# Kernel tuning notes

Hardware: AMD Instinct MI355X
Metric: run time of the kernel (lower is better)

Reference implementation:

```python
import jax, jax.numpy as jnp
import numpy as np

EMBED = 1024
HEADS = 16
HEAD_DIM = EMBED // HEADS
FF = 4096
LN_EPS = 1e-5


def _layer_norm(x, scale, bias):
    mu = jnp.mean(x, axis=-1, keepdims=True)
    var = jnp.mean(jnp.square(x - mu), axis=-1, keepdims=True)
    return (x - mu) * jax.lax.rsqrt(var + LN_EPS) * scale + bias


def setup_inputs() -> dict:
    key = jax.random.key(0)
    ks = jax.random.split(key, 16)
    B, T, CARRY = 8, 128, 4096
    s = 0.02
    return {
        "hidden": jax.random.normal(ks[0], (B, T, EMBED), jnp.float32),
        "key_carry": jax.random.normal(ks[1], (B, HEADS, CARRY, HEAD_DIM), jnp.float32),
        "value_carry": jax.random.normal(ks[2], (B, HEADS, CARRY, HEAD_DIM), jnp.float32),
        "ln1_scale": jnp.ones((EMBED,), jnp.float32),
        "ln1_bias": jnp.zeros((EMBED,), jnp.float32),
        "wq": jax.random.normal(ks[3], (EMBED, EMBED), jnp.float32) * s,
        "bq": jnp.zeros((EMBED,), jnp.float32),
        "wk": jax.random.normal(ks[4], (EMBED, EMBED), jnp.float32) * s,
        "bk": jnp.zeros((EMBED,), jnp.float32),
        "wv": jax.random.normal(ks[5], (EMBED, EMBED), jnp.float32) * s,
        "bv": jnp.zeros((EMBED,), jnp.float32),
        "wo": jax.random.normal(ks[6], (EMBED, EMBED), jnp.float32) * s,
        "bo": jnp.zeros((EMBED,), jnp.float32),
        "ln2_scale": jnp.ones((EMBED,), jnp.float32),
        "ln2_bias": jnp.zeros((EMBED,), jnp.float32),
        "w1": jax.random.normal(ks[7], (EMBED, FF), jnp.float32) * s,
        "b1": jnp.zeros((FF,), jnp.float32),
        "w2": jax.random.normal(ks[8], (FF, EMBED), jnp.float32) * s,
        "b2": jnp.zeros((EMBED,), jnp.float32),
    }


def reference(hidden, key_carry, value_carry, ln1_scale, ln1_bias, wq, bq, wk, bk,
              wv, bv, wo, bo, ln2_scale, ln2_bias, w1, b1, w2, b2):
    B, T, _ = hidden.shape
    carry_len = key_carry.shape[2]

    x = _layer_norm(hidden, ln1_scale, ln1_bias)
    # [B, H, T, Dh]
    def split_heads(y):
        return y.reshape(B, T, HEADS, HEAD_DIM).transpose(0, 2, 1, 3)
    q = split_heads(x @ wq + bq)
    k = split_heads(x @ wk + bk)
    v = split_heads(x @ wv + bv)

    k_all = jnp.concatenate([key_carry, k], axis=2)   # [B,H,C+T,Dh]
    v_all = jnp.concatenate([value_carry, v], axis=2)

    scores = jnp.einsum("bhtd,bhsd->bhts", q, k_all) / jnp.sqrt(jnp.float32(HEAD_DIM))
    kv_pos = jnp.arange(carry_len + T)
    q_pos = jnp.arange(T)[:, None] + carry_len
    causal = kv_pos[None, :] <= q_pos  # [T, C+T]
    scores = jnp.where(causal[None, None], scores, jnp.float32(-jnp.inf))
    attn = jax.nn.softmax(scores, axis=-1)  # dropout=0.0 (eval)
    ctx = jnp.einsum("bhts,bhsd->bhtd", attn, v_all)
    ctx = ctx.transpose(0, 2, 1, 3).reshape(B, T, EMBED)
    hidden = hidden + (ctx @ wo + bo)

    f = _layer_norm(hidden, ln2_scale, ln2_bias)
    f = jax.nn.gelu(f @ w1 + b1, approximate=False) @ w2 + b2
    hidden = hidden + f
    return hidden, k_all, v_all
```

## Files before the change

kernel.cpp:

```cpp
#include <hip/hip_runtime.h>
#include <hip/hip_bf16.h>
#include <math.h>

#define EMBED 1024
#define HEADS 16
#define HDIM 64
#define FFDIM 4096
#define BATCH 8
#define TLEN 128
#define CARRY 4096
#define SEQA (CARRY + TLEN)
#define MROWS (BATCH * TLEN)
#define NSPLIT 8

typedef __attribute__((ext_vector_type(8))) short bf16x8;
typedef __attribute__((ext_vector_type(4))) float f32x4;
typedef unsigned short u16;

static __device__ __forceinline__ u16 f2b(float v) {
    __hip_bfloat16 h = __float2bfloat16(v);
    return *reinterpret_cast<u16*>(&h);
}

typedef const __attribute__((address_space(1))) unsigned int g_u32;
// ... 109 lines not shown
        float4 v = *(const float4*)(W + (size_t)(k0 + r) * N + n0 + c);
        Ls[r][c] = v.x; Ls[r][c + 1] = v.y; Ls[r][c + 2] = v.z; Ls[r][c + 3] = v.w;
    }
    __syncthreads();
#pragma unroll
    for (int p = 0; p < 4; p++) {
        int n = (tid >> 4) + 16 * p, k4 = (tid & 15) * 4;
        u16 o0 = f2b(Ls[k4][n]), o1 = f2b(Ls[k4 + 1][n]);
        u16 o2 = f2b(Ls[k4 + 2][n]), o3 = f2b(Ls[k4 + 3][n]);
        unsigned int a = (unsigned int)o0 | ((unsigned int)o1 << 16);
        unsigned int b = (unsigned int)o2 | ((unsigned int)o3 << 16);
        uint2 pk = {a, b};
        *(uint2*)(WT + (size_t)(n0 + n) * K + k0 + k4) = pk;
    }
}

static __device__ __forceinline__ void stage2(const u16* __restrict__ Ag,
                                              const u16* __restrict__ Wg,
                                              u16* As, u16* Ws,
                                              int w, int l, int K) {
    int r0 = 16 * w + (l >> 3);
    int scol = ((l & 7) ^ (l >> 3)) * 8;
    char* a0 = (char*)As + w * 2048;
    char* w0 = (char*)Ws + w * 2048;
    gl16(Ag + (size_t)r0 * K + scol, a0);
    gl16(Ag + (size_t)(r0 + 8) * K + scol, a0 + 1024);
    gl16(Wg + (size_t)r0 * K + scol, w0);
    gl16(Wg + (size_t)(r0 + 8) * K + scol, w0 + 1024);
}

template <int MODE>
__global__ __launch_bounds__(256) void gemm_bf16(const u16* __restrict__ A,
                                                 const u16* __restrict__ WT,
                                                 const float* __restrict__ bias,
                                                 const float* __restrict__ resid,
                                                 float* __restrict__ outf,
                                                 float* __restrict__ outf2,
                                                 u16* __restrict__ outb, int N, int K) {
    __shared__ u16 As[64 * 64];
    __shared__ u16 Ws[64 * 64];
    int tid = threadIdx.x;
    int m0 = blockIdx.y * 64, n0 = blockIdx.x * 64;
    int w = tid >> 6, l = tid & 63, lr = l & 15, lg = l >> 4;
    f32x4 acc[4] = {};

    const u16* Ag = A + (size_t)m0 * K;
    const u16* Wg = WT + (size_t)n0 * K;

    for (int k0 = 0; k0 < K; k0 += 64) {
        __syncthreads();
        stage2(Ag + k0, Wg + k0, As, Ws, w, l, K);
        __syncthreads();
#pragma unroll
        for (int ks = 0; ks < 2; ks++) {
            int abyte = ((16 * w + lr) * 128 + lg * 16 + ks * 64) ^ ((lr & 7) << 4);
            bf16x8 af = *(bf16x8*)((char*)As + abyte);
#pragma unroll
            for (int f = 0; f < 4; f++) {
                int bbyte = ((16 * f + lr) * 128 + lg * 16 + ks * 64) ^ ((lr & 7) << 4);
                bf16x8 bfr = *(bf16x8*)((char*)Ws + bbyte);
                acc[f] = __builtin_amdgcn_mfma_f32_16x16x32_bf16(af, bfr, acc[f], 0, 0, 0);
            }
        }
    }

    int gr0 = m0 + 16 * w + 4 * lg;
#pragma unroll
    for (int f = 0; f < 4; f++) {
        int gc = n0 + 16 * f + lr;
        float bv = bias[gc];
#pragma unroll
        for (int r = 0; r < 4; r++) {
            int gm = gr0 + r;
            float v = acc[f][r] + bv;
            if (MODE == 3) v = 0.5f * v * (1.0f + erff(v * 0.70710678118654752f));
            if (MODE == 2 || MODE == 4) v += resid[(size_t)gm * EMBED + gc];
            if (MODE == 0 || MODE == 3) {
                outb[(size_t)gm * N + gc] = f2b(v);
            } else if (MODE == 1) {
                int b_ = gm >> 7, t_ = gm & 127, h_ = gc >> 6, d_ = gc & 63;
                outf[(((size_t)(b_ * HEADS + h_)) * SEQA + CARRY + t_) * HDIM + d_] = v;
            } else if (MODE == 5) {
                if (gc < 1024) {
                    outb[(size_t)gm * EMBED + gc] = f2b(v);
                } else {
                    int which = gc >> 10;
                    int gc2 = gc & 1023;
                    int b_ = gm >> 7, t_ = gm & 127, h_ = gc2 >> 6, d_ = gc2 & 63;
                    float* dst = (which == 1) ? outf : outf2;
                    dst[(((size_t)(b_ * HEADS + h_)) * SEQA + CARRY + t_) * HDIM + d_] = v;
                }
            } else {
                outf[(size_t)gm * EMBED + gc] = v;
            }
        }
    }
}

__global__ __launch_bounds__(256) void gemm_splitk(const u16* __restrict__ A,
                                                   const u16* __restrict__ WT,
                                                   float* __restrict__ part,
                                                   int N, int Ktot, int Klen) {
    __shared__ u16 As[64 * 64];
    __shared__ u16 Ws[64 * 64];
    int tid = threadIdx.x;
    int m0 = blockIdx.y * 64, n0 = blockIdx.x * 64;
    int k0s = blockIdx.z * Klen;
    int w = tid >> 6, l = tid & 63, lr = l & 15, lg = l >> 4;
    f32x4 acc[4] = {};

    const u16* Ag = A + (size_t)m0 * Ktot;
    const u16* Wg = WT + (size_t)n0 * Ktot;

    for (int k0 = k0s; k0 < k0s + Klen; k0 += 64) {
        __syncthreads();
        stage2(Ag + k0, Wg + k0, As, Ws, w, l, Ktot);
        __syncthreads();
#pragma unroll
        for (int ks = 0; ks < 2; ks++) {
            int abyte = ((16 * w + lr) * 128 + lg * 16 + ks * 64) ^ ((lr & 7) << 4);
            bf16x8 af = *(bf16x8*)((char*)As + abyte);
#pragma unroll
            for (int f = 0; f < 4; f++) {
                int bbyte = ((16 * f + lr) * 128 + lg * 16 + ks * 64) ^ ((lr & 7) << 4);
                bf16x8 bfr = *(bf16x8*)((char*)Ws + bbyte);
                acc[f] = __builtin_amdgcn_mfma_f32_16x16x32_bf16(af, bfr, acc[f], 0, 0, 0);
            }
        }
    }

    float* pbase = part + (size_t)blockIdx.z * MROWS * N;
    int gr0 = m0 + 16 * w + 4 * lg;
#pragma unroll
    for (int f = 0; f < 4; f++) {
        int gc = n0 + 16 * f + lr;
#pragma unroll
        for (int r = 0; r < 4; r++)
            pbase[(size_t)(gr0 + r) * N + gc] = acc[f][r];
    }
}

template <int NS>
__global__ __launch_bounds__(256) void combine_add(const float* __restrict__ part,
                                                   const float* __restrict__ bias,
                                                   const float* __restrict__ resid,
                                                   float* __restrict__ out) {
    size_t e = ((size_t)blockIdx.x * 256 + threadIdx.x) * 4;
    int n0 = (int)(e & 1023);
    float4 v = *(const float4*)(resid + e);
    float4 b = *(const float4*)(bias + n0);
    v.x += b.x; v.y += b.y; v.z += b.z; v.w += b.w;
#pragma unroll
    for (int s = 0; s < NS; s++) {
        float4 p = *(const float4*)(part + (size_t)s * MROWS * EMBED + e);
        v.x += p.x; v.y += p.y; v.z += p.z; v.w += p.w;
    }
    *(float4*)(out + e) = v;
}

__global__ __launch_bounds__(256) void combine_ln(const float* __restrict__ part,
                                                  const float* __restrict__ bias,
                                                  const float* __restrict__ resid,
                                                  const float* __restrict__ ln_s,
                                                  const float* __restrict__ ln_b,
                                                  float* __restrict__ out,
                                                  u16* __restrict__ outb) {
    int row = blockIdx.x, tid = threadIdx.x;
    size_t base = (size_t)row * EMBED + tid * 4;
    float4 v = *(const float4*)(resid + base);
    float4 b = *(const float4*)(bias + tid * 4);
    v.x += b.x; v.y += b.y; v.z += b.z; v.w += b.w;
#pragma unroll
    for (int s = 0; s < 2; s++) {
        float4 p = *(const float4*)(part + (size_t)s * MROWS * EMBED + base);
        v.x += p.x; v.y += p.y; v.z += p.z; v.w += p.w;
    }
    *(float4*)(out + base) = v;

    float s1 = v.x + v.y + v.z + v.w;
    float s2 = v.x * v.x + v.y * v.y + v.z * v.z + v.w * v.w;
    for (int o = 32; o > 0; o >>= 1) {
        s1 += __shfl_down(s1, o, 64);
        s2 += __shfl_down(s2, o, 64);
    }
    __shared__ float ls[8], ls2[8];
    int wid = tid >> 6, lane = tid & 63;
    if (lane == 0) { ls[wid] = s1; ls2[wid] = s2; }
    __syncthreads();
    if (tid == 0) {
        float S = 0.f, S2 = 0.f;
        for (int i = 0; i < 4; i++) { S += ls[i]; S2 += ls2[i]; }
        float mu = S * (1.0f / EMBED);
        float var = S2 * (1.0f / EMBED) - mu * mu;
        ls[0] = mu;
        ls2[0] = rsqrtf(var + 1e-5f);
    }
    __syncthreads();
    float mu = ls[0], rstd = ls2[0];
    float sc[4], bi[4];
    *(float4*)sc = ((const float4*)ln_s)[tid];
    *(float4*)bi = ((const float4*)ln_b)[tid];
    u16 o0 = f2b((v.x - mu) * rstd * sc[0] + bi[0]);
    u16 o1 = f2b((v.y - mu) * rstd * sc[1] + bi[1]);
    u16 o2 = f2b((v.z - mu) * rstd * sc[2] + bi[2]);
    u16 o3 = f2b((v.w - mu) * rstd * sc[3] + bi[3]);
    unsigned int u0 = (unsigned int)o0 | ((unsigned int)o1 << 16);
    unsigned int u1 = (unsigned int)o2 | ((unsigned int)o3 << 16);
    uint2 pk = {u0, u1};
    *(uint2*)(outb + base) = pk;
}

__global__ __launch_bounds__(256) void attn_mfma_split(const u16* __restrict__ qb,
                                                       const float* __restrict__ kc,
                                                       const float* __restrict__ vc,
                                                       float* __restrict__ k_all,
                                                       float* __restrict__ v_all,
                                                       float* __restrict__ part_acc,
                                                       float* __restrict__ part_m,
                                                       float* __restrict__ part_l) {
    __shared__ u16 Ks[64 * 64];
    __shared__ u16 Vt[64 * 64];
    __shared__ u16 Ps[64 * 64];

    int bh = blockIdx.x, b = bh >> 4, h = bh & 15;
    int qh = blockIdx.y;
    int q0 = qh * 64;
    int sp = blockIdx.z;
    int tid = threadIdx.x;
    int w = tid >> 6, l = tid & 63, lr = l & 15, lg = l >> 4;
    const bool WR = (qh == 0);

    bf16x8 qf0, qf1;
    {
        const u16* qrow = qb + (size_t)(b * TLEN + q0 + 16 * w + lr) * EMBED + h * HDIM;
        qf0 = *(const bf16x8*)(qrow + 8 * lg);
        qf1 = *(const bf16x8*)(qrow + 8 * lg + 32);
    }

    const float* kcb = kc + (size_t)bh * CARRY * HDIM;
    const float* vcb = vc + (size_t)bh * CARRY * HDIM;
    const float* kb = k_all + (size_t)bh * SEQA * HDIM;
    const float* vb = v_all + (size_t)bh * SEQA * HDIM;
    float* kwr = k_all + (size_t)bh * SEQA * HDIM;
    float* vwr = v_all + (size_t)bh * SEQA * HDIM;

    float m_run[4], l_run[4];
    f32x4 oacc[4] = {};
#pragma unroll
    for (int r = 0; r < 4; r++) { m_run[r] = -1e30f; l_run[r] = 0.f; }

    int nt = (CARRY + q0 + 64) >> 6;
    int tps = (nt + NSPLIT - 1) / NSPLIT;
    int kt0 = sp * tps;
    int kt1 = min(kt0 + tps, nt);

    int krow = tid >> 4;
    int vrow4 = (tid >> 4) * 4;
    int col = (tid & 15) * 4;

    float4 kA[4], vA[4], kB[4], vB[4];

    {
        bool cn = kt0 < 64;
        const float* ksrc = cn ? kcb : kb;
        const float* vsrc = cn ? vcb : vb;
#pragma unroll
        for (int p = 0; p < 4; p++)
            kA[p] = *(const float4*)(ksrc + (size_t)(kt0 * 64 + krow + 16 * p) * HDIM + col);
#pragma unroll
        for (int p = 0; p < 4; p++)
            vA[p] = *(const float4*)(vsrc + (size_t)(kt0 * 64 + vrow4 + p) * HDIM + col);
    }

    auto body = [&](float4 (&kc_)[4], float4 (&vc_)[4],
                    float4 (&kn_)[4], float4 (&vn_)[4], int kt) {
        bool carry_t = kt < 64;
        int ktn = kt + 1;
        if (ktn < kt1) {
            bool cn = ktn < 64;
            const float* ksrc = cn ? kcb : kb;
            const float* vsrc = cn ? vcb : vb;
#pragma unroll
            for (int p = 0; p < 4; p++)
                kn_[p] = *(const float4*)(ksrc + (size_t)(ktn * 64 + krow + 16 * p) * HDIM + col);
#pragma unroll
            for (int p = 0; p < 4; p++)
                vn_[p] = *(const float4*)(vsrc + (size_t)(ktn * 64 + vrow4 + p) * HDIM + col);
        }
        if (WR && carry_t) {
#pragma unroll
            for (int p = 0; p < 4; p++)
                *(float4*)(kwr + (size_t)(kt * 64 + krow + 16 * p) * HDIM + col) = kc_[p];
#pragma unroll
            for (int p = 0; p < 4; p++)
                *(float4*)(vwr + (size_t)(kt * 64 + vrow4 + p) * HDIM + col) = vc_[p];
        }
        bar_plain();
#pragma unroll
        for (int p = 0; p < 4; p++) {
            int s = krow + 16 * p;
            u16 t0 = f2b(kc_[p].x), t1 = f2b(kc_[p].y), t2 = f2b(kc_[p].z), t3 = f2b(kc_[p].w);
            unsigned int a = (unsigned int)t0 | ((unsigned int)t1 << 16);
            unsigned int bq = (unsigned int)t2 | ((unsigned int)t3 << 16);
            uint2 pk = {a, bq};
            *(uint2*)((char*)Ks + ((s * 128 + col * 2) ^ ((s & 7) << 4))) = pk;
        }
#pragma unroll
        for (int i = 0; i < 4; i++) {
            int d = col + i;
            u16 e0 = f2b(((const float*)&vc_[0])[i]);
            u16 e1 = f2b(((const float*)&vc_[1])[i]);
            u16 e2 = f2b(((const float*)&vc_[2])[i]);
            u16 e3 = f2b(((const float*)&vc_[3])[i]);
            unsigned int a = (unsigned int)e0 | ((unsigned int)e1 << 16);
            unsigned int bq = (unsigned int)e2 | ((unsigned int)e3 << 16);
            uint2 pk = {a, bq};
            *(uint2*)((char*)Vt + ((d * 128 + vrow4 * 2) ^ ((d & 7) << 4))) = pk;
        }
        bar_lgkm();

        float x[4][4];
#pragma unroll
        for (int f = 0; f < 4; f++) {
            int row = 16 * f + lr;
            int swz = (row & 7) << 4;
            bf16x8 kf0 = *(bf16x8*)((char*)Ks + ((row * 128 + 16 * lg) ^ swz));
            bf16x8 kf1 = *(bf16x8*)((char*)Ks + ((row * 128 + 16 * lg + 64) ^ swz));
            f32x4 z = {};
            z = __builtin_amdgcn_mfma_f32_16x16x32_bf16(qf0, kf0, z, 0, 0, 0);
            z = __builtin_amdgcn_mfma_f32_16x16x32_bf16(qf1, kf1, z, 0, 0, 0);
#pragma unroll
            for (int r = 0; r < 4; r++) x[f][r] = z[r] * 0.125f;
        }
        if (kt * 64 + 63 > CARRY + q0 + 16 * w) {
#pragma unroll
            for (int f = 0; f < 4; f++) {
                int sg = kt * 64 + 16 * f + lr;
#pragma unroll
                for (int r = 0; r < 4; r++) {
                    int tg = q0 + 16 * w + 4 * lg + r;
                    if (sg > CARRY + tg) x[f][r] = -1e30f;
                }
            }
        }
#pragma unroll
        for (int r = 0; r < 4; r++) {
            float mt = fmaxf(fmaxf(x[0][r], x[1][r]), fmaxf(x[2][r], x[3][r]));
            mt = fmaxf(mt, __shfl_xor(mt, 1, 64));
            mt = fmaxf(mt, __shfl_xor(mt, 2, 64));
            mt = fmaxf(mt, __shfl_xor(mt, 4, 64));
            mt = fmaxf(mt, __shfl_xor(mt, 8, 64));
            float mn = fmaxf(m_run[r], mt);
            float fs = __expf(m_run[r] - mn);
            m_run[r] = mn;
            float s = 0.f;
#pragma unroll
            for (int f = 0; f < 4; f++) {
                float p = __expf(x[f][r] - mn);
                x[f][r] = p;
                s += p;
            }
            s += __shfl_xor(s, 1, 64);
            s += __shfl_xor(s, 2, 64);
            s += __shfl_xor(s, 4, 64);
            s += __shfl_xor(s, 8, 64);
            l_run[r] = l_run[r] * fs + s;
#pragma unroll
            for (int f2 = 0; f2 < 4; f2++) oacc[f2][r] *= fs;
        }
#pragma unroll
        for (int f = 0; f < 4; f++) {
#pragma unroll
            for (int r = 0; r < 4; r++) {
                int row = 16 * w + 4 * lg + r;
                int byte = (row * 128 + (16 * f + lr) * 2) ^ ((row & 7) << 4);
                *(u16*)((char*)Ps + byte) = f2b(x[f][r]);
            }
        }
        {
            int prow = 16 * w + lr;
            int pswz = (prow & 7) << 4;
            bf16x8 pa0 = *(bf16x8*)((char*)Ps + ((prow * 128 + 16 * lg) ^ pswz));
            bf16x8 pa1 = *(bf16x8*)((char*)Ps + ((prow * 128 + 16 * lg + 64) ^ pswz));
#pragma unroll
            for (int f2 = 0; f2 < 4; f2++) {
                int d = 16 * f2 + lr;
                int vswz = (d & 7) << 4;
                bf16x8 vf0 = *(bf16x8*)((char*)Vt + ((d * 128 + 16 * lg) ^ vswz));
                bf16x8 vf1 = *(bf16x8*)((char*)Vt + ((d * 128 + 16 * lg + 64) ^ vswz));
                oacc[f2] = __builtin_amdgcn_mfma_f32_16x16x32_bf16(pa0, vf0, oacc[f2], 0, 0, 0);
                oacc[f2] = __builtin_amdgcn_mfma_f32_16x16x32_bf16(pa1, vf1, oacc[f2], 0, 0, 0);
            }
        }
    };

    for (int kt = kt0; kt < kt1; kt += 2) {
        body(kA, vA, kB, vB, kt);
        if (kt + 1 < kt1) body(kB, vB, kA, vA, kt + 1);
    }

    int p = (bh * 2 + qh) * NSPLIT + sp;
    if (lr == 0) {
#pragma unroll
        for (int r = 0; r < 4; r++) {
            int row = 16 * w + 4 * lg + r;
            part_m[(size_t)p * 64 + row] = m_run[r];
            part_l[(size_t)p * 64 + row] = l_run[r];
        }
    }
#pragma unroll
    for (int f2 = 0; f2 < 4; f2++) {
#pragma unroll
        for (int r = 0; r < 4; r++) {
            int row = 16 * w + 4 * lg + r;
            part_acc[(size_t)p * 4096 + row * 64 + 16 * f2 + lr] = oacc[f2][r];
        }
    }
}

__global__ __launch_bounds__(256) void attn_combine(const float* __restrict__ part_acc,
                                                    const float* __restrict__ part_m,
                                                    const float* __restrict__ part_l,
                                                    u16* __restrict__ ctx) {
    int g = blockIdx.x;
    int bh = g >> 1, qh = g & 1, b = bh >> 4, h = bh & 15;
    int t = threadIdx.x;
    int r = t >> 2, c0 = (t & 3) * 16;
    int p0 = g * NSPLIT;

    float ms[NSPLIT];
    float M = -1e30f;
#pragma unroll
    for (int s = 0; s < NSPLIT; s++) {
        ms[s] = part_m[(size_t)(p0 + s) * 64 + r];
        M = fmaxf(M, ms[s]);
    }
    float wgt[NSPLIT];
    float L = 0.f;
#pragma unroll
    for (int s = 0; s < NSPLIT; s++) {
        wgt[s] = __expf(ms[s] - M);
        L += wgt[s] * part_l[(size_t)(p0 + s) * 64 + r];
    }
    float inv = 1.0f / L;

    size_t grow = (size_t)(b * TLEN + qh * 64 + r) * EMBED + h * HDIM + c0;
#pragma unroll
    for (int j = 0; j < 16; j += 4) {
        float4 a = {0.f, 0.f, 0.f, 0.f};
#pragma unroll
        for (int s = 0; s < NSPLIT; s++) {
            float4 p = *(const float4*)(part_acc + (size_t)(p0 + s) * 4096 + r * 64 + c0 + j);
            a.x += wgt[s] * p.x; a.y += wgt[s] * p.y; a.z += wgt[s] * p.z; a.w += wgt[s] * p.w;
        }
        u16 o0 = f2b(a.x * inv), o1 = f2b(a.y * inv), o2 = f2b(a.z * inv), o3 = f2b(a.w * inv);
        unsigned int u0 = (unsigned int)o0 | ((unsigned int)o1 << 16);
        unsigned int u1 = (unsigned int)o2 | ((unsigned int)o3 << 16);
        uint2 pk = {u0, u1};
        *(uint2*)(ctx + grow + j) = pk;
    }
}

__global__ __launch_bounds__(256) void attn_mfma(const u16* __restrict__ qb,
                                                 const float* __restrict__ k_all,
                                                 const float* __restrict__ v_all,
                                                 u16* __restrict__ ctx) {
    __shared__ u16 Ks[64 * 64];
    __shared__ u16 Vt[64 * 64];
    __shared__ u16 Ps[64 * 64];

    int bh = blockIdx.x, b = bh >> 4, h = bh & 15;
    int q0 = blockIdx.y * 64;
    int tid = threadIdx.x;
    int w = tid >> 6, l = tid & 63, lr = l & 15, lg = l >> 4;

    bf16x8 qf0, qf1;
    {
        const u16* qrow = qb + (size_t)(b * TLEN + q0 + 16 * w + lr) * EMBED + h * HDIM;
        qf0 = *(const bf16x8*)(qrow + 8 * lg);
        qf1 = *(const bf16x8*)(qrow + 8 * lg + 32);
    }
    const float* kb = k_all + (size_t)bh * SEQA * HDIM;
    const float* vb = v_all + (size_t)bh * SEQA * HDIM;

    float m_run[4], l_run[4];
    f32x4 oacc[4] = {};
#pragma unroll
    for (int r = 0; r < 4; r++) { m_run[r] = -1e30f; l_run[r] = 0.f; }

    int nt = (CARRY + q0 + 64) >> 6;
    for (int kt = 0; kt < nt; kt++) {
        __syncthreads();
#pragma unroll
        for (int p = 0; p < 4; p++) {
            int s = (tid >> 4) + 16 * p, c = (tid & 15) * 4;
            float4 kv = *(const float4*)(kb + (size_t)(kt * 64 + s) * HDIM + c);
            u16 t0 = f2b(kv.x), t1 = f2b(kv.y), t2 = f2b(kv.z), t3 = f2b(kv.w);
            unsigned int a = (unsigned int)t0 | ((unsigned int)t1 << 16);
            unsigned int bq = (unsigned int)t2 | ((unsigned int)t3 << 16);
            uint2 pk = {a, bq};
            int byte = (s * 128 + c * 2) ^ ((s & 7) << 4);
            *(uint2*)((char*)Ks + byte) = pk;
        }
        {
            int d = tid & 63;
            u16 tmp[16];
#pragma unroll
            for (int q = 0; q < 16; q++)
                tmp[q] = f2b(vb[(size_t)(kt * 64 + 16 * w + q) * HDIM + d]);
            int b0 = (d * 128 + 32 * w) ^ ((d & 7) << 4);
            int b1 = (d * 128 + 32 * w + 16) ^ ((d & 7) << 4);
            *(bf16x8*)((char*)Vt + b0) = *(bf16x8*)&tmp[0];
            *(bf16x8*)((char*)Vt + b1) = *(bf16x8*)&tmp[8];
        }
        __syncthreads();

        float x[4][4];
#pragma unroll
        for (int f = 0; f < 4; f++) {
            int row = 16 * f + lr;
            int swz = (row & 7) << 4;
            bf16x8 kf0 = *(bf16x8*)((char*)Ks + ((row * 128 + 16 * lg) ^ swz));
            bf16x8 kf1 = *(bf16x8*)((char*)Ks + ((row * 128 + 16 * lg + 64) ^ swz));
            f32x4 z = {};
            z = __builtin_amdgcn_mfma_f32_16x16x32_bf16(qf0, kf0, z, 0, 0, 0);
            z = __builtin_amdgcn_mfma_f32_16x16x32_bf16(qf1, kf1, z, 0, 0, 0);
#pragma unroll
            for (int r = 0; r < 4; r++) x[f][r] = z[r] * 0.125f;
        }
        if (kt * 64 + 63 > CARRY + q0 + 16 * w) {
#pragma unroll
            for (int f = 0; f < 4; f++) {
                int sg = kt * 64 + 16 * f + lr;
#pragma unroll
                for (int r = 0; r < 4; r++) {
// ... 21 lines not shown
            }
            s += __shfl_xor(s, 1, 64);
            s += __shfl_xor(s, 2, 64);
            s += __shfl_xor(s, 4, 64);
            s += __shfl_xor(s, 8, 64);
            l_run[r] = l_run[r] * fs + s;
#pragma unroll
            for (int f2 = 0; f2 < 4; f2++) oacc[f2][r] *= fs;
        }
#pragma unroll
        for (int f = 0; f < 4; f++) {
#pragma unroll
            for (int r = 0; r < 4; r++) {
                int row = 16 * w + 4 * lg + r;
                int byte = (row * 128 + (16 * f + lr) * 2) ^ ((row & 7) << 4);
                *(u16*)((char*)Ps + byte) = f2b(x[f][r]);
            }
        }
        {
            int prow = 16 * w + lr;
            int pswz = (prow & 7) << 4;
            bf16x8 pa0 = *(bf16x8*)((char*)Ps + ((prow * 128 + 16 * lg) ^ pswz));
            bf16x8 pa1 = *(bf16x8*)((char*)Ps + ((prow * 128 + 16 * lg + 64) ^ pswz));
#pragma unroll
            for (int f2 = 0; f2 < 4; f2++) {
                int d = 16 * f2 + lr;
                int vswz = (d & 7) << 4;
                bf16x8 vf0 = *(bf16x8*)((char*)Vt + ((d * 128 + 16 * lg) ^ vswz));
                bf16x8 vf1 = *(bf16x8*)((char*)Vt + ((d * 128 + 16 * lg + 64) ^ vswz));
                oacc[f2] = __builtin_amdgcn_mfma_f32_16x16x32_bf16(pa0, vf0, oacc[f2], 0, 0, 0);
                oacc[f2] = __builtin_amdgcn_mfma_f32_16x16x32_bf16(pa1, vf1, oacc[f2], 0, 0, 0);
            }
        }
    }
#pragma unroll
    for (int r = 0; r < 4; r++) {
        float inv = 1.0f / l_run[r];
        size_t grow = (size_t)(b * TLEN + q0 + 16 * w + 4 * lg + r) * EMBED + h * HDIM;
#pragma unroll
        for (int f2 = 0; f2 < 4; f2++)
            ctx[grow + 16 * f2 + lr] = f2b(oacc[f2][r] * inv);
    }
}

extern "C" void kernel_launch(void* const* d_in, const int* in_sizes, int n_in,
                              void* d_out, int out_size, void* d_ws, size_t ws_size,
                              hipStream_t stream) {
    const float* hidden = (const float*)d_in[0];
    const float* key_carry = (const float*)d_in[1];
    const float* value_carry = (const float*)d_in[2];
    const float* ln1_s = (const float*)d_in[3];
    const float* ln1_b = (const float*)d_in[4];
    const float* wq = (const float*)d_in[5];
    const float* bq = (const float*)d_in[6];
    const float* wk = (const float*)d_in[7];
    const float* bk = (const float*)d_in[8];
    const float* wv = (const float*)d_in[9];
    const float* bv = (const float*)d_in[10];
    const float* wo = (const float*)d_in[11];
    const float* bo = (const float*)d_in[12];
    const float* ln2_s = (const float*)d_in[13];
    const float* ln2_b = (const float*)d_in[14];
    const float* w1 = (const float*)d_in[15];
    const float* b1 = (const float*)d_in[16];
    const float* w2 = (const float*)d_in[17];
    const float* b2 = (const float*)d_in[18];

    float* out_hidden = (float*)d_out;
    float* k_all = out_hidden + (size_t)MROWS * EMBED;
    float* v_all = k_all + (size_t)BATCH * HEADS * SEQA * HDIM;

    u16* wsu = (u16*)d_ws;
    u16* wqkvT = wsu;
    u16* woT = wsu + 3145728;
    u16* w1T = wsu + 4194304;
    u16* w2T = wsu + 8388608;
    u16* xb  = wsu + 12582912;
    u16* qbb = wsu + 13631488;
    u16* ctxb = wsu + 14680064;
    u16* fb  = wsu + 15728640;
    u16* h1b = wsu + 16777216;
    float* bias_qkv = (float*)(wsu + 20971520);
    float* part = (float*)(wsu + 20977664);
    const size_t nparts = (size_t)256 * NSPLIT;
    const size_t need = (size_t)20977664 * 2 +
                        (nparts * 4096 + 2 * nparts * 64) * 4;

    transpose_all<<<dim3(16, 16, 12), 256, 0, stream>>>(wq, wk, wv, wo, w1, w2, bq, bk, bv,
                                                        wqkvT, woT, w1T, w2T, bias_qkv);

    ln_kernel<<<MROWS, 256, 0, stream>>>(hidden, ln1_s, ln1_b, xb);

    if (ws_size >= need) {
        gemm_bf16<5><<<dim3(48, 16), 256, 0, stream>>>(xb, wqkvT, bias_qkv, nullptr,
                                                       k_all, v_all, qbb, 3072, EMBED);
        float* part_acc = part;
        float* part_m = part + nparts * 4096;
        float* part_l = part_m + nparts * 64;
        attn_mfma_split<<<dim3(BATCH * HEADS, 2, NSPLIT), 256, 0, stream>>>(
            qbb, key_carry, value_carry, k_all, v_all, part_acc, part_m, part_l);
        attn_combine<<<256, 256, 0, stream>>>(part_acc, part_m, part_l, ctxb);

        gemm_splitk<<<dim3(16, 16, 2), 256, 0, stream>>>(ctxb, woT, part, EMBED, EMBED, 512);
        combine_ln<<<1024, 256, 0, stream>>>(part, bo, hidden, ln2_s, ln2_b, out_hidden, fb);

        gemm_bf16<3><<<dim3(64, 16), 256, 0, stream>>>(fb, w1T, b1, nullptr, nullptr, nullptr,
                                                       h1b, FFDIM, EMBED);
        gemm_splitk<<<dim3(16, 16, 4), 256, 0, stream>>>(h1b, w2T, part, EMBED, FFDIM, 1024);
        combine_add<4><<<1024, 256, 0, stream>>>(part, b2, out_hidden, out_hidden);
    } else {
        copy_carry_kernel<<<2048, 256, 0, stream>>>(
            (const float4*)key_carry, (const float4*)value_carry,
            (float4*)k_all, (float4*)v_all);
        u16* wqT = wqkvT;
        u16* wkT = wqkvT + 1048576;
        u16* wvT = wqkvT + 2097152;
        gemm_bf16<0><<<dim3(16, 16), 256, 0, stream>>>(xb, wqT, bq, nullptr, nullptr, nullptr,
                                                       qbb, EMBED, EMBED);
        gemm_bf16<1><<<dim3(16, 16), 256, 0, stream>>>(xb, wkT, bk, nullptr, k_all, nullptr,
                                                       nullptr, EMBED, EMBED);
        gemm_bf16<1><<<dim3(16, 16), 256, 0, stream>>>(xb, wvT, bv, nullptr, v_all, nullptr,
                                                       nullptr, EMBED, EMBED);
        attn_mfma<<<dim3(BATCH * HEADS, 2), 256, 0, stream>>>(qbb, k_all, v_all, ctxb);
        gemm_bf16<2><<<dim3(16, 16), 256, 0, stream>>>(ctxb, woT, bo, hidden, out_hidden,
                                                       nullptr, nullptr, EMBED, EMBED);
        ln_kernel<<<MROWS, 256, 0, stream>>>(out_hidden, ln2_s, ln2_b, fb);
        gemm_bf16<3><<<dim3(64, 16), 256, 0, stream>>>(fb, w1T, b1, nullptr, nullptr, nullptr,
                                                       h1b, FFDIM, EMBED);
        gemm_bf16<4><<<dim3(16, 16), 256, 0, stream>>>(h1b, w2T, b2, out_hidden, out_hidden,
                                                       nullptr, nullptr, EMBED, FFDIM);
    }
}
```

Measured before the change: 251.3 us.

## Process all 128 query rows per attention block to halve K/V loads

Result: slower. 289.0 us (+15.0%).

```diff
diff --git a/kernel.cpp b/kernel.cpp
--- a/kernel.cpp
+++ b/kernel.cpp
@@ -353,21 +353,19 @@
                                                        float* __restrict__ part_l) {
     __shared__ u16 Ks[64 * 64];
     __shared__ u16 Vt[64 * 64];
-    __shared__ u16 Ps[64 * 64];
+    __shared__ u16 Ps[128 * 64];
 
     int bh = blockIdx.x, b = bh >> 4, h = bh & 15;
-    int qh = blockIdx.y;
-    int q0 = qh * 64;
-    int sp = blockIdx.z;
+    int sp = blockIdx.y;
     int tid = threadIdx.x;
     int w = tid >> 6, l = tid & 63, lr = l & 15, lg = l >> 4;
-    const bool WR = (qh == 0);
-
-    bf16x8 qf0, qf1;
-    {
-        const u16* qrow = qb + (size_t)(b * TLEN + q0 + 16 * w + lr) * EMBED + h * HDIM;
-        qf0 = *(const bf16x8*)(qrow + 8 * lg);
-        qf1 = *(const bf16x8*)(qrow + 8 * lg + 32);
+
+    bf16x8 qf[2][2];
+#pragma unroll
+    for (int rr = 0; rr < 2; rr++) {
+        const u16* qrow = qb + (size_t)(b * TLEN + 32 * w + 16 * rr + lr) * EMBED + h * HDIM;
+        qf[rr][0] = *(const bf16x8*)(qrow + 8 * lg);
+        qf[rr][1] = *(const bf16x8*)(qrow + 8 * lg + 32);
     }
 
     const float* kcb = kc + (size_t)bh * CARRY * HDIM;
@@ -377,13 +375,15 @@
     float* kwr = k_all + (size_t)bh * SEQA * HDIM;
     float* vwr = v_all + (size_t)bh * SEQA * HDIM;
 
-    float m_run[4], l_run[4];
-    f32x4 oacc[4] = {};
-#pragma unroll
-    for (int r = 0; r < 4; r++) { m_run[r] = -1e30f; l_run[r] = 0.f; }
-
-    int nt = (CARRY + q0 + 64) >> 6;
-    int tps = (nt + NSPLIT - 1) / NSPLIT;
+    float m_run[2][4], l_run[2][4];
+    f32x4 oacc[2][4] = {};
+#pragma unroll
+    for (int rr = 0; rr < 2; rr++)
+#pragma unroll
+        for (int r = 0; r < 4; r++) { m_run[rr][r] = -1e30f; l_run[rr][r] = 0.f; }
+
+    const int nt = SEQA / 64;
+    const int tps = (nt + NSPLIT - 1) / NSPLIT;
     int kt0 = sp * tps;
     int kt1 = min(kt0 + tps, nt);
 
@@ -420,7 +420,7 @@
             for (int p = 0; p < 4; p++)
                 vn_[p] = *(const float4*)(vsrc + (size_t)(ktn * 64 + vrow4 + p) * HDIM + col);
         }
-        if (WR && carry_t) {
+        if (carry_t) {
 #pragma unroll
             for (int p = 0; p < 4; p++)
                 *(float4*)(kwr + (size_t)(kt * 64 + krow + 16 * p) * HDIM + col) = kc_[p];
@@ -452,66 +452,70 @@
         }
         bar_lgkm();
 
-        float x[4][4];
-#pragma unroll
-        for (int f = 0; f < 4; f++) {
-            int row = 16 * f + lr;
-            int swz = (row & 7) << 4;
-            bf16x8 kf0 = *(bf16x8*)((char*)Ks + ((row * 128 + 16 * lg) ^ swz));
-            bf16x8 kf1 = *(bf16x8*)((char*)Ks + ((row * 128 + 16 * lg + 64) ^ swz));
-            f32x4 z = {};
-            z = __builtin_amdgcn_mfma_f32_16x16x32_bf16(qf0, kf0, z, 0, 0, 0);
-            z = __builtin_amdgcn_mfma_f32_16x16x32_bf16(qf1, kf1, z, 0, 0, 0);
-#pragma unroll
-            for (int r = 0; r < 4; r++) x[f][r] = z[r] * 0.125f;
-        }
-        if (kt * 64 + 63 > CARRY + q0 + 16 * w) {
+#pragma unroll
+        for (int rr = 0; rr < 2; rr++) {
+            float x[4][4];
 #pragma unroll
             for (int f = 0; f < 4; f++) {
-                int sg = kt * 64 + 16 * f + lr;
+                int row = 16 * f + lr;
+                int swz = (row & 7) << 4;
+                bf16x8 kf0 = *(bf16x8*)((char*)Ks + ((row * 128 + 16 * lg) ^ swz));
+                bf16x8 kf1 = *(bf16x8*)((char*)Ks + ((row * 128 + 16 * lg + 64) ^ swz));
+                f32x4 z = {};
+                z = __builtin_amdgcn_mfma_f32_16x16x32_bf16(qf[rr][0], kf0, z, 0, 0, 0);
+                z = __builtin_amdgcn_mfma_f32_16x16x32_bf16(qf[rr][1], kf1, z, 0, 0, 0);
+#pragma unroll
+                for (int r = 0; r < 4; r++) x[f][r] = z[r] * 0.125f;
+            }
+            if (kt * 64 + 63 > CARRY + 32 * w + 16 * rr) {
+#pragma unroll
+                for (int f = 0; f < 4; f++) {
+                    int sg = kt * 64 + 16 * f + lr;
+#pragma unroll
+                    for (int r = 0; r < 4; r++) {
+                        int tg = 32 * w + 16 * rr + 4 * lg + r;
+                        if (sg > CARRY + tg) x[f][r] = -1e30f;
+                    }
+                }
+            }
+#pragma unroll
+            for (int r = 0; r < 4; r++) {
+                float mt = fmaxf(fmaxf(x[0][r], x[1][r]), fmaxf(x[2][r], x[3][r]));
+                mt = fmaxf(mt, __shfl_xor(mt, 1, 64));
+                mt = fmaxf(mt, __shfl_xor(mt, 2, 64));
+                mt = fmaxf(mt, __shfl_xor(mt, 4, 64));
+                mt = fmaxf(mt, __shfl_xor(mt, 8, 64));
+                float mn = fmaxf(m_run[rr][r], mt);
+                float fs = __expf(m_run[rr][r] - mn);
+                m_run[rr][r] = mn;
+                float s = 0.f;
+#pragma unroll
+                for (int f = 0; f < 4; f++) {
+                    float p = __expf(x[f][r] - mn);
+                    x[f][r] = p;
+                    s += p;
+                }
+                s += __shfl_xor(s, 1, 64);
+                s += __shfl_xor(s, 2, 64);
+                s += __shfl_xor(s, 4, 64);
+                s += __shfl_xor(s, 8, 64);
+                l_run[rr][r] = l_run[rr][r] * fs + s;
+#pragma unroll
+                for (int f2 = 0; f2 < 4; f2++) oacc[rr][f2][r] *= fs;
+            }
+#pragma unroll
+            for (int f = 0; f < 4; f++) {
 #pragma unroll
                 for (int r = 0; r < 4; r++) {
-                    int tg = q0 + 16 * w + 4 * lg + r;
-                    if (sg > CARRY + tg) x[f][r] = -1e30f;
+                    int row = 32 * w + 16 * rr + 4 * lg + r;
+                    int byte = (row * 128 + (16 * f + lr) * 2) ^ ((row & 7) << 4);
+                    *(u16*)((char*)Ps + byte) = f2b(x[f][r]);
                 }
             }
         }
 #pragma unroll
-        for (int r = 0; r < 4; r++) {
-            float mt = fmaxf(fmaxf(x[0][r], x[1][r]), fmaxf(x[2][r], x[3][r]));
-            mt = fmaxf(mt, __shfl_xor(mt, 1, 64));
-            mt = fmaxf(mt, __shfl_xor(mt, 2, 64));
-            mt = fmaxf(mt, __shfl_xor(mt, 4, 64));
-            mt = fmaxf(mt, __shfl_xor(mt, 8, 64));
-            float mn = fmaxf(m_run[r], mt);
-            float fs = __expf(m_run[r] - mn);
-            m_run[r] = mn;
-            float s = 0.f;
-#pragma unroll
-            for (int f = 0; f < 4; f++) {
-                float p = __expf(x[f][r] - mn);
-                x[f][r] = p;
-                s += p;
-            }
-            s += __shfl_xor(s, 1, 64);
-            s += __shfl_xor(s, 2, 64);
-            s += __shfl_xor(s, 4, 64);
-            s += __shfl_xor(s, 8, 64);
-            l_run[r] = l_run[r] * fs + s;
-#pragma unroll
-            for (int f2 = 0; f2 < 4; f2++) oacc[f2][r] *= fs;
-        }
-#pragma unroll
-        for (int f = 0; f < 4; f++) {
-#pragma unroll
-            for (int r = 0; r < 4; r++) {
-                int row = 16 * w + 4 * lg + r;
-                int byte = (row * 128 + (16 * f + lr) * 2) ^ ((row & 7) << 4);
-                *(u16*)((char*)Ps + byte) = f2b(x[f][r]);
-            }
-        }
-        {
-            int prow = 16 * w + lr;
+        for (int rr = 0; rr < 2; rr++) {
+            int prow = 32 * w + 16 * rr + lr;
             int pswz = (prow & 7) << 4;
             bf16x8 pa0 = *(bf16x8*)((char*)Ps + ((prow * 128 + 16 * lg) ^ pswz));
             bf16x8 pa1 = *(bf16x8*)((char*)Ps + ((prow * 128 + 16 * lg + 64) ^ pswz));
@@ -521,8 +525,8 @@
                 int vswz = (d & 7) << 4;
                 bf16x8 vf0 = *(bf16x8*)((char*)Vt + ((d * 128 + 16 * lg) ^ vswz));
                 bf16x8 vf1 = *(bf16x8*)((char*)Vt + ((d * 128 + 16 * lg + 64) ^ vswz));
-                oacc[f2] = __builtin_amdgcn_mfma_f32_16x16x32_bf16(pa0, vf0, oacc[f2], 0, 0, 0);
-                oacc[f2] = __builtin_amdgcn_mfma_f32_16x16x32_bf16(pa1, vf1, oacc[f2], 0, 0, 0);
+                oacc[rr][f2] = __builtin_amdgcn_mfma_f32_16x16x32_bf16(pa0, vf0, oacc[rr][f2], 0, 0, 0);
+                oacc[rr][f2] = __builtin_amdgcn_mfma_f32_16x16x32_bf16(pa1, vf1, oacc[rr][f2], 0, 0, 0);
             }
         }
     };
@@ -532,21 +536,24 @@
         if (kt + 1 < kt1) body(kB, vB, kA, vA, kt + 1);
     }
 
-    int p = (bh * 2 + qh) * NSPLIT + sp;
-    if (lr == 0) {
-#pragma unroll
-        for (int r = 0; r < 4; r++) {
-            int row = 16 * w + 4 * lg + r;
-            part_m[(size_t)p * 64 + row] = m_run[r];
-            part_l[(size_t)p * 64 + row] = l_run[r];
-        }
-    }
-#pragma unroll
-    for (int f2 = 0; f2 < 4; f2++) {
-#pragma unroll
-        for (int r = 0; r < 4; r++) {
-            int row = 16 * w + 4 * lg + r;
-            part_acc[(size_t)p * 4096 + row * 64 + 16 * f2 + lr] = oacc[f2][r];
+    int p = bh * NSPLIT + sp;
+#pragma unroll
+    for (int rr = 0; rr < 2; rr++) {
+        if (lr == 0) {
+#pragma unroll
+            for (int r = 0; r < 4; r++) {
+                int row = 32 * w + 16 * rr + 4 * lg + r;
+                part_m[(size_t)p * 128 + row] = m_run[rr][r];
+                part_l[(size_t)p * 128 + row] = l_run[rr][r];
+            }
+        }
+#pragma unroll
+        for (int f2 = 0; f2 < 4; f2++) {
+#pragma unroll
+            for (int r = 0; r < 4; r++) {
+                int row = 32 * w + 16 * rr + 4 * lg + r;
+                part_acc[(size_t)p * 8192 + row * 64 + 16 * f2 + lr] = oacc[rr][f2][r];
+            }
         }
     }
 }
@@ -559,13 +566,14 @@
     int bh = g >> 1, qh = g & 1, b = bh >> 4, h = bh & 15;
     int t = threadIdx.x;
     int r = t >> 2, c0 = (t & 3) * 16;
-    int p0 = g * NSPLIT;
+    int row = qh * 64 + r;
+    int p0 = bh * NSPLIT;
 
     float ms[NSPLIT];
     float M = -1e30f;
 #pragma unroll
     for (int s = 0; s < NSPLIT; s++) {
-        ms[s] = part_m[(size_t)(p0 + s) * 64 + r];
+        ms[s] = part_m[(size_t)(p0 + s) * 128 + row];
         M = fmaxf(M, ms[s]);
     }
     float wgt[NSPLIT];
@@ -573,17 +581,17 @@
 #pragma unroll
     for (int s = 0; s < NSPLIT; s++) {
         wgt[s] = __expf(ms[s] - M);
-        L += wgt[s] * part_l[(size_t)(p0 + s) * 64 + r];
+        L += wgt[s] * part_l[(size_t)(p0 + s) * 128 + row];
     }
     float inv = 1.0f / L;
 
-    size_t grow = (size_t)(b * TLEN + qh * 64 + r) * EMBED + h * HDIM + c0;
+    size_t grow = (size_t)(b * TLEN + row) * EMBED + h * HDIM + c0;
 #pragma unroll
     for (int j = 0; j < 16; j += 4) {
         float4 a = {0.f, 0.f, 0.f, 0.f};
 #pragma unroll
         for (int s = 0; s < NSPLIT; s++) {
-            float4 p = *(const float4*)(part_acc + (size_t)(p0 + s) * 4096 + r * 64 + c0 + j);
+            float4 p = *(const float4*)(part_acc + (size_t)(p0 + s) * 8192 + row * 64 + c0 + j);
             a.x += wgt[s] * p.x; a.y += wgt[s] * p.y; a.z += wgt[s] * p.z; a.w += wgt[s] * p.w;
         }
         u16 o0 = f2b(a.x * inv), o1 = f2b(a.y * inv), o2 = f2b(a.z * inv), o3 = f2b(a.w * inv);
@@ -771,9 +779,9 @@
     u16* h1b = wsu + 16777216;
     float* bias_qkv = (float*)(wsu + 20971520);
     float* part = (float*)(wsu + 20977664);
-    const size_t nparts = (size_t)256 * NSPLIT;
+    const size_t nparts = (size_t)128 * NSPLIT;
     const size_t need = (size_t)20977664 * 2 +
-                        (nparts * 4096 + 2 * nparts * 64) * 4;
+                        (nparts * 8192 + 2 * nparts * 128) * 4;
 
     transpose_all<<<dim3(16, 16, 12), 256, 0, stream>>>(wq, wk, wv, wo, w1, w2, bq, bk, bv,
                                                         wqkvT, woT, w1T, w2T, bias_qkv);
@@ -784,9 +792,9 @@
         gemm_bf16<5><<<dim3(48, 16), 256, 0, stream>>>(xb, wqkvT, bias_qkv, nullptr,
                                                        k_all, v_all, qbb, 3072, EMBED);
         float* part_acc = part;
-        float* part_m = part + nparts * 4096;
-        float* part_l = part_m + nparts * 64;
-        attn_mfma_split<<<dim3(BATCH * HEADS, 2, NSPLIT), 256, 0, stream>>>(
+        float* part_m = part + nparts * 8192;
+        float* part_l = part_m + nparts * 128;
+        attn_mfma_split<<<dim3(BATCH * HEADS, NSPLIT), 256, 0, stream>>>(
             qbb, key_carry, value_carry, k_all, v_all, part_acc, part_m, part_l);
         attn_combine<<<256, 256, 0, stream>>>(part_acc, part_m, part_l, ctxb);
 
```

## Merge both query halves into one 512-thread attention block per split

Applied to the files above, without the earlier changes.

Result: slower. 316.8 us (+26.0%).

```diff
diff --git a/kernel.cpp b/kernel.cpp
--- a/kernel.cpp
+++ b/kernel.cpp
@@ -343,29 +343,26 @@
     *(uint2*)(outb + base) = pk;
 }
 
-__global__ __launch_bounds__(256) void attn_mfma_split(const u16* __restrict__ qb,
-                                                       const float* __restrict__ kc,
-                                                       const float* __restrict__ vc,
-                                                       float* __restrict__ k_all,
-                                                       float* __restrict__ v_all,
-                                                       float* __restrict__ part_acc,
-                                                       float* __restrict__ part_m,
-                                                       float* __restrict__ part_l) {
+__global__ __launch_bounds__(512, 4) void attn_mfma_split(const u16* __restrict__ qb,
+                                                          const float* __restrict__ kc,
+                                                          const float* __restrict__ vc,
+                                                          float* __restrict__ k_all,
+                                                          float* __restrict__ v_all,
+                                                          float* __restrict__ part_acc,
+                                                          float* __restrict__ part_m,
+                                                          float* __restrict__ part_l) {
     __shared__ u16 Ks[64 * 64];
     __shared__ u16 Vt[64 * 64];
-    __shared__ u16 Ps[64 * 64];
+    __shared__ u16 Ps[128 * 64];
 
     int bh = blockIdx.x, b = bh >> 4, h = bh & 15;
-    int qh = blockIdx.y;
-    int q0 = qh * 64;
-    int sp = blockIdx.z;
+    int sp = blockIdx.y;
     int tid = threadIdx.x;
     int w = tid >> 6, l = tid & 63, lr = l & 15, lg = l >> 4;
-    const bool WR = (qh == 0);
 
     bf16x8 qf0, qf1;
     {
-        const u16* qrow = qb + (size_t)(b * TLEN + q0 + 16 * w + lr) * EMBED + h * HDIM;
+        const u16* qrow = qb + (size_t)(b * TLEN + 16 * w + lr) * EMBED + h * HDIM;
         qf0 = *(const bf16x8*)(qrow + 8 * lg);
         qf1 = *(const bf16x8*)(qrow + 8 * lg + 32);
     }
@@ -382,73 +379,65 @@
 #pragma unroll
     for (int r = 0; r < 4; r++) { m_run[r] = -1e30f; l_run[r] = 0.f; }
 
-    int nt = (CARRY + q0 + 64) >> 6;
-    int tps = (nt + NSPLIT - 1) / NSPLIT;
+    const int nt = SEQA / 64;
+    const int tps = (nt + NSPLIT - 1) / NSPLIT;
     int kt0 = sp * tps;
     int kt1 = min(kt0 + tps, nt);
 
-    int krow = tid >> 4;
-    int vrow4 = (tid >> 4) * 4;
-    int col = (tid & 15) * 4;
-
-    float4 kA[4], vA[4], kB[4], vB[4];
+    int krow = tid >> 3;
+    int kcol = (tid & 7) * 8;
+    int vs0 = 8 * w;
+
+    float4 kA[2], kB[2];
+    float vA[8], vB[8];
 
     {
         bool cn = kt0 < 64;
         const float* ksrc = cn ? kcb : kb;
         const float* vsrc = cn ? vcb : vb;
-#pragma unroll
-        for (int p = 0; p < 4; p++)
-            kA[p] = *(const float4*)(ksrc + (size_t)(kt0 * 64 + krow + 16 * p) * HDIM + col);
-#pragma unroll
-        for (int p = 0; p < 4; p++)
-            vA[p] = *(const float4*)(vsrc + (size_t)(kt0 * 64 + vrow4 + p) * HDIM + col);
-    }
-
-    auto body = [&](float4 (&kc_)[4], float4 (&vc_)[4],
-                    float4 (&kn_)[4], float4 (&vn_)[4], int kt) {
+        kA[0] = *(const float4*)(ksrc + (size_t)(kt0 * 64 + krow) * HDIM + kcol);
+        kA[1] = *(const float4*)(ksrc + (size_t)(kt0 * 64 + krow) * HDIM + kcol + 4);
+#pragma unroll
+        for (int q = 0; q < 8; q++)
+            vA[q] = vsrc[(size_t)(kt0 * 64 + vs0 + q) * HDIM + l];
+    }
+
+    auto body = [&](float4 (&kc_)[2], float (&vc_)[8],
+                    float4 (&kn_)[2], float (&vn_)[8], int kt) {
         bool carry_t = kt < 64;
         int ktn = kt + 1;
         if (ktn < kt1) {
             bool cn = ktn < 64;
             const float* ksrc = cn ? kcb : kb;
             const float* vsrc = cn ? vcb : vb;
-#pragma unroll
-            for (int p = 0; p < 4; p++)
-                kn_[p] = *(const float4*)(ksrc + (size_t)(ktn * 64 + krow + 16 * p) * HDIM + col);
-#pragma unroll
-            for (int p = 0; p < 4; p++)
-                vn_[p] = *(const float4*)(vsrc + (size_t)(ktn * 64 + vrow4 + p) * HDIM + col);
-        }
-        if (WR && carry_t) {
-#pragma unroll
-            for (int p = 0; p < 4; p++)
-                *(float4*)(kwr + (size_t)(kt * 64 + krow + 16 * p) * HDIM + col) = kc_[p];
-#pragma unroll
-            for (int p = 0; p < 4; p++)
-                *(float4*)(vwr + (size_t)(kt * 64 + vrow4 + p) * HDIM + col) = vc_[p];
+            kn_[0] = *(const float4*)(ksrc + (size_t)(ktn * 64 + krow) * HDIM + kcol);
+            kn_[1] = *(const float4*)(ksrc + (size_t)(ktn * 64 + krow) * HDIM + kcol + 4);
+#pragma unroll
+            for (int q = 0; q < 8; q++)
+                vn_[q] = vsrc[(size_t)(ktn * 64 + vs0 + q) * HDIM + l];
+        }
+        if (carry_t) {
+            *(float4*)(kwr + (size_t)(kt * 64 + krow) * HDIM + kcol) = kc_[0];
+            *(float4*)(kwr + (size_t)(kt * 64 + krow) * HDIM + kcol + 4) = kc_[1];
+#pragma unroll
+            for (int q = 0; q < 8; q++)
+                vwr[(size_t)(kt * 64 + vs0 + q) * HDIM + l] = vc_[q];
         }
         bar_plain();
-#pragma unroll
-        for (int p = 0; p < 4; p++) {
-            int s = krow + 16 * p;
-            u16 t0 = f2b(kc_[p].x), t1 = f2b(kc_[p].y), t2 = f2b(kc_[p].z), t3 = f2b(kc_[p].w);
-            unsigned int a = (unsigned int)t0 | ((unsigned int)t1 << 16);
-            unsigned int bq = (unsigned int)t2 | ((unsigned int)t3 << 16);
-            uint2 pk = {a, bq};
-            *(uint2*)((char*)Ks + ((s * 128 + col * 2) ^ ((s & 7) << 4))) = pk;
-        }
-#pragma unroll
-        for (int i = 0; i < 4; i++) {
-            int d = col + i;
-            u16 e0 = f2b(((const float*)&vc_[0])[i]);
-            u16 e1 = f2b(((const float*)&vc_[1])[i]);
-            u16 e2 = f2b(((const float*)&vc_[2])[i]);
-            u16 e3 = f2b(((const float*)&vc_[3])[i]);
-            unsigned int a = (unsigned int)e0 | ((unsigned int)e1 << 16);
-            unsigned int bq = (unsigned int)e2 | ((unsigned int)e3 << 16);
-            uint2 pk = {a, bq};
-            *(uint2*)((char*)Vt + ((d * 128 + vrow4 * 2) ^ ((d & 7) << 4))) = pk;
+        {
+            u16 t[8];
+            const float* kf = (const float*)&kc_[0];
+#pragma unroll
+            for (int j = 0; j < 8; j++) t[j] = f2b(kf[j]);
+            *(bf16x8*)((char*)Ks + ((krow * 128 + kcol * 2) ^ ((krow & 7) << 4))) =
+                *(bf16x8*)t;
+        }
+        {
+            u16 t[8];
+#pragma unroll
+            for (int q = 0; q < 8; q++) t[q] = f2b(vc_[q]);
+            *(bf16x8*)((char*)Vt + ((l * 128 + vs0 * 2) ^ ((l & 7) << 4))) =
+                *(bf16x8*)t;
         }
         bar_lgkm();
 
@@ -465,13 +454,13 @@
 #pragma unroll
             for (int r = 0; r < 4; r++) x[f][r] = z[r] * 0.125f;
         }
-        if (kt * 64 + 63 > CARRY + q0 + 16 * w) {
+        if (kt * 64 + 63 > CARRY + 16 * w) {
 #pragma unroll
             for (int f = 0; f < 4; f++) {
                 int sg = kt * 64 + 16 * f + lr;
 #pragma unroll
                 for (int r = 0; r < 4; r++) {
-                    int tg = q0 + 16 * w + 4 * lg + r;
+                    int tg = 16 * w + 4 * lg + r;
                     if (sg > CARRY + tg) x[f][r] = -1e30f;
                 }
             }
@@ -532,13 +521,13 @@
         if (kt + 1 < kt1) body(kB, vB, kA, vA, kt + 1);
     }
 
-    int p = (bh * 2 + qh) * NSPLIT + sp;
+    int p = bh * NSPLIT + sp;
     if (lr == 0) {
 #pragma unroll
         for (int r = 0; r < 4; r++) {
             int row = 16 * w + 4 * lg + r;
-            part_m[(size_t)p * 64 + row] = m_run[r];
-            part_l[(size_t)p * 64 + row] = l_run[r];
+            part_m[(size_t)p * 128 + row] = m_run[r];
+            part_l[(size_t)p * 128 + row] = l_run[r];
         }
     }
 #pragma unroll
@@ -546,7 +535,7 @@
 #pragma unroll
         for (int r = 0; r < 4; r++) {
             int row = 16 * w + 4 * lg + r;
-            part_acc[(size_t)p * 4096 + row * 64 + 16 * f2 + lr] = oacc[f2][r];
+            part_acc[(size_t)p * 8192 + row * 64 + 16 * f2 + lr] = oacc[f2][r];
         }
     }
 }
@@ -559,13 +548,14 @@
     int bh = g >> 1, qh = g & 1, b = bh >> 4, h = bh & 15;
     int t = threadIdx.x;
     int r = t >> 2, c0 = (t & 3) * 16;
-    int p0 = g * NSPLIT;
+    int row = qh * 64 + r;
+    int p0 = bh * NSPLIT;
 
     float ms[NSPLIT];
     float M = -1e30f;
 #pragma unroll
     for (int s = 0; s < NSPLIT; s++) {
-        ms[s] = part_m[(size_t)(p0 + s) * 64 + r];
+        ms[s] = part_m[(size_t)(p0 + s) * 128 + row];
         M = fmaxf(M, ms[s]);
     }
     float wgt[NSPLIT];
@@ -573,17 +563,17 @@
 #pragma unroll
     for (int s = 0; s < NSPLIT; s++) {
         wgt[s] = __expf(ms[s] - M);
-        L += wgt[s] * part_l[(size_t)(p0 + s) * 64 + r];
+        L += wgt[s] * part_l[(size_t)(p0 + s) * 128 + row];
     }
     float inv = 1.0f / L;
 
-    size_t grow = (size_t)(b * TLEN + qh * 64 + r) * EMBED + h * HDIM + c0;
+    size_t grow = (size_t)(b * TLEN + row) * EMBED + h * HDIM + c0;
 #pragma unroll
     for (int j = 0; j < 16; j += 4) {
         float4 a = {0.f, 0.f, 0.f, 0.f};
 #pragma unroll
         for (int s = 0; s < NSPLIT; s++) {
-            float4 p = *(const float4*)(part_acc + (size_t)(p0 + s) * 4096 + r * 64 + c0 + j);
+            float4 p = *(const float4*)(part_acc + (size_t)(p0 + s) * 8192 + row * 64 + c0 + j);
             a.x += wgt[s] * p.x; a.y += wgt[s] * p.y; a.z += wgt[s] * p.z; a.w += wgt[s] * p.w;
         }
         u16 o0 = f2b(a.x * inv), o1 = f2b(a.y * inv), o2 = f2b(a.z * inv), o3 = f2b(a.w * inv);
@@ -771,9 +761,9 @@
     u16* h1b = wsu + 16777216;
     float* bias_qkv = (float*)(wsu + 20971520);
     float* part = (float*)(wsu + 20977664);
-    const size_t nparts = (size_t)256 * NSPLIT;
+    const size_t nparts = (size_t)128 * NSPLIT;
     const size_t need = (size_t)20977664 * 2 +
-                        (nparts * 4096 + 2 * nparts * 64) * 4;
+                        (nparts * 8192 + 2 * nparts * 128) * 4;
 
     transpose_all<<<dim3(16, 16, 12), 256, 0, stream>>>(wq, wk, wv, wo, w1, w2, bq, bk, bv,
                                                         wqkvT, woT, w1T, w2T, bias_qkv);
@@ -784,9 +774,9 @@
         gemm_bf16<5><<<dim3(48, 16), 256, 0, stream>>>(xb, wqkvT, bias_qkv, nullptr,
                                                        k_all, v_all, qbb, 3072, EMBED);
         float* part_acc = part;
-        float* part_m = part + nparts * 4096;
-        float* part_l = part_m + nparts * 64;
-        attn_mfma_split<<<dim3(BATCH * HEADS, 2, NSPLIT), 256, 0, stream>>>(
+        float* part_m = part + nparts * 8192;
+        float* part_l = part_m + nparts * 128;
+        attn_mfma_split<<<dim3(BATCH * HEADS, NSPLIT), 512, 0, stream>>>(
             qbb, key_carry, value_carry, k_all, v_all, part_acc, part_m, part_l);
         attn_combine<<<256, 256, 0, stream>>>(part_acc, part_m, part_l, ctxb);
 
```

## Lazy softmax rescaling, fold scale into Q, MFMA row sums

Applied to the files above, without the earlier changes.

Result: faster. 243.6 us (-3.1%).

```diff
diff --git a/kernel.cpp b/kernel.cpp
--- a/kernel.cpp
+++ b/kernel.cpp
@@ -215,7 +215,7 @@
                 outf[(((size_t)(b_ * HEADS + h_)) * SEQA + CARRY + t_) * HDIM + d_] = v;
             } else if (MODE == 5) {
                 if (gc < 1024) {
-                    outb[(size_t)gm * EMBED + gc] = f2b(v);
+                    outb[(size_t)gm * EMBED + gc] = f2b(v * 0.125f);
                 } else {
                     int which = gc >> 10;
                     int gc2 = gc & 1023;
@@ -370,6 +370,10 @@
         qf1 = *(const bf16x8*)(qrow + 8 * lg + 32);
     }
 
+    bf16x8 onesf;
+#pragma unroll
+    for (int j = 0; j < 8; j++) onesf[j] = (short)0x3F80;
+
     const float* kcb = kc + (size_t)bh * CARRY * HDIM;
     const float* vcb = vc + (size_t)bh * CARRY * HDIM;
     const float* kb = k_all + (size_t)bh * SEQA * HDIM;
@@ -377,10 +381,11 @@
     float* kwr = k_all + (size_t)bh * SEQA * HDIM;
     float* vwr = v_all + (size_t)bh * SEQA * HDIM;
 
-    float m_run[4], l_run[4];
+    float m_run[4];
+    f32x4 lacc = {};
     f32x4 oacc[4] = {};
 #pragma unroll
-    for (int r = 0; r < 4; r++) { m_run[r] = -1e30f; l_run[r] = 0.f; }
+    for (int r = 0; r < 4; r++) m_run[r] = -1e30f;
 
     int nt = (CARRY + q0 + 64) >> 6;
     int tps = (nt + NSPLIT - 1) / NSPLIT;
@@ -463,7 +468,7 @@
             z = __builtin_amdgcn_mfma_f32_16x16x32_bf16(qf0, kf0, z, 0, 0, 0);
             z = __builtin_amdgcn_mfma_f32_16x16x32_bf16(qf1, kf1, z, 0, 0, 0);
 #pragma unroll
-            for (int r = 0; r < 4; r++) x[f][r] = z[r] * 0.125f;
+            for (int r = 0; r < 4; r++) x[f][r] = z[r];
         }
         if (kt * 64 + 63 > CARRY + q0 + 16 * w) {
 #pragma unroll
@@ -476,31 +481,33 @@
                 }
             }
         }
-#pragma unroll
-        for (int r = 0; r < 4; r++) {
-            float mt = fmaxf(fmaxf(x[0][r], x[1][r]), fmaxf(x[2][r], x[3][r]));
-            mt = fmaxf(mt, __shfl_xor(mt, 1, 64));
-            mt = fmaxf(mt, __shfl_xor(mt, 2, 64));
-            mt = fmaxf(mt, __shfl_xor(mt, 4, 64));
-            mt = fmaxf(mt, __shfl_xor(mt, 8, 64));
-            float mn = fmaxf(m_run[r], mt);
-            float fs = __expf(m_run[r] - mn);
-            m_run[r] = mn;
-            float s = 0.f;
-#pragma unroll
-            for (int f = 0; f < 4; f++) {
-                float p = __expf(x[f][r] - mn);
-                x[f][r] = p;
-                s += p;
-            }
-            s += __shfl_xor(s, 1, 64);
-            s += __shfl_xor(s, 2, 64);
-            s += __shfl_xor(s, 4, 64);
-            s += __shfl_xor(s, 8, 64);
-            l_run[r] = l_run[r] * fs + s;
-#pragma unroll
-            for (int f2 = 0; f2 < 4; f2++) oacc[f2][r] *= fs;
-        }
+        float lm[4];
+#pragma unroll
+        for (int r = 0; r < 4; r++)
+            lm[r] = fmaxf(fmaxf(x[0][r], x[1][r]), fmaxf(x[2][r], x[3][r]));
+        bool need = __any(lm[0] > m_run[0] + 8.f) || __any(lm[1] > m_run[1] + 8.f) ||
+                    __any(lm[2] > m_run[2] + 8.f) || __any(lm[3] > m_run[3] + 8.f);
+        if (need) {
+#pragma unroll
+            for (int r = 0; r < 4; r++) {
+                float mt = lm[r];
+                mt = fmaxf(mt, __shfl_xor(mt, 1, 64));
+                mt = fmaxf(mt, __shfl_xor(mt, 2, 64));
+                mt = fmaxf(mt, __shfl_xor(mt, 4, 64));
+                mt = fmaxf(mt, __shfl_xor(mt, 8, 64));
+                float mn = fmaxf(m_run[r], mt);
+                float fs = __expf(m_run[r] - mn);
+                m_run[r] = mn;
+                lacc[r] *= fs;
+#pragma unroll
+                for (int f2 = 0; f2 < 4; f2++) oacc[f2][r] *= fs;
+            }
+        }
+#pragma unroll
+        for (int f = 0; f < 4; f++)
+#pragma unroll
+            for (int r = 0; r < 4; r++)
+                x[f][r] = __expf(x[f][r] - m_run[r]);
 #pragma unroll
         for (int f = 0; f < 4; f++) {
 #pragma unroll
@@ -515,6 +522,8 @@
             int pswz = (prow & 7) << 4;
             bf16x8 pa0 = *(bf16x8*)((char*)Ps + ((prow * 128 + 16 * lg) ^ pswz));
             bf16x8 pa1 = *(bf16x8*)((char*)Ps + ((prow * 128 + 16 * lg + 64) ^ pswz));
+            lacc = __builtin_amdgcn_mfma_f32_16x16x32_bf16(pa0, onesf, lacc, 0, 0, 0);
+            lacc = __builtin_amdgcn_mfma_f32_16x16x32_bf16(pa1, onesf, lacc, 0, 0, 0);
 #pragma unroll
             for (int f2 = 0; f2 < 4; f2++) {
                 int d = 16 * f2 + lr;
@@ -538,7 +547,7 @@
         for (int r = 0; r < 4; r++) {
             int row = 16 * w + 4 * lg + r;
             part_m[(size_t)p * 64 + row] = m_run[r];
-            part_l[(size_t)p * 64 + row] = l_run[r];
+            part_l[(size_t)p * 64 + row] = lacc[r];
         }
     }
 #pragma unroll
```
